# Performance work log

Measured on AMD Instinct MI355X. Metric: run time of the kernel, lower is better.

Reference implementation:

```python
import jax, jax.numpy as jnp
import numpy as np

HIDDEN = 256
ACTIONS = 8
FEAT = 256
N, T = 64, 1024


def _orthogonal(key, shape, scale):
    # hk.initializers.Orthogonal(sqrt(2)) equivalent
    n_rows, n_cols = shape
    big = max(n_rows, n_cols)
    m = jax.random.normal(key, (big, big), dtype=jnp.float32)
    q, r = jnp.linalg.qr(m)
    q = q * jnp.sign(jnp.diag(r))
    return scale * q[:n_rows, :n_cols]


def setup_inputs() -> dict:
    key = jax.random.key(0)
    ks = jax.random.split(key, 8)
    x = jax.random.normal(ks[0], (N, T, FEAT), dtype=jnp.float32)
    a = jax.random.normal(ks[1], (N, T, ACTIONS), dtype=jnp.float32)
    reset = jax.random.randint(ks[2], (N, T), 0, 2).astype(bool)
    s = np.sqrt(2).astype(np.float32)
    w_i = _orthogonal(ks[3], (FEAT, 3 * HIDDEN), s)
    w_h = _orthogonal(ks[4], (HIDDEN, 3 * HIDDEN), s)
    w_a = _orthogonal(ks[5], (ACTIONS, 3 * HIDDEN), s)
    b = jnp.zeros((3 * HIDDEN,), dtype=jnp.float32)
    initial_h = jnp.zeros((HIDDEN,), dtype=jnp.float32)
    return {"x": x, "a": a, "reset": reset, "w_i": w_i, "w_h": w_h,
            "w_a": w_a, "b": b, "initial_h": initial_h}


def reference(x, a, reset, w_i, w_h, w_a, b, initial_h):
    # x: [N,T,F], a: [N,T,A] (one-hot-like), reset: [N,T] bool
    H = initial_h.shape[0]
    w_h_z, w_h_a = w_h[:, :2 * H], w_h[:, 2 * H:]
    b_z, b_a = b[:2 * H], b[2 * H:]
    # Input-side gate projections are time-independent: precompute once.
    gx = jnp.einsum('ntf,fg->ntg', x, w_i)  # [N,T,3H]
    ga = jnp.einsum('nta,ag->ntg', a, w_a)  # [N,T,3H]
    n = x.shape[0]
    h0 = jnp.broadcast_to(initial_h[None, :], (n, H))

    def step(h, inp):
        gx_t, ga_t, r_t = inp  # [N,3H], [N,3H], [N]
        # carry sequence equals learned initial_h (learn_initial_h, is_target=False,
        # carry=None path), so reset restores the learned initial state.
        h = jnp.where(r_t[:, None], initial_h[None, :], h)
        zr = gx_t[:, :2 * H] + ga_t[:, :2 * H] + h @ w_h_z + b_z
        z, r = jnp.split(jax.nn.sigmoid(zr), 2, axis=-1)
        a_t = jnp.tanh(gx_t[:, 2 * H:] + ga_t[:, 2 * H:] + (r * h) @ w_h_a + b_a)
        h_next = (1.0 - z) * h + z * a_t
        return h_next, h_next

    xs = (jnp.swapaxes(gx, 0, 1), jnp.swapaxes(ga, 0, 1), jnp.swapaxes(reset, 0, 1))
    _, hs = jax.lax.scan(step, h0, xs)  # hs: [T,N,H]
    states = jnp.swapaxes(hs, 0, 1)     # [N,T,H]
    outputs = states                    # gru_call returns (next_state, next_state)
    return outputs, states, initial_h[None, :]
```

## Files before the change

kernel.cpp:

```cpp
#include <hip/hip_runtime.h>
#include <hip/hip_fp16.h>

#define NB 64
#define TT 1024
#define FF 256
#define HH 256
#define GG 768
#define AA 8
#define KP 288
#define MM (NB*TT)
#define SGRP 16
#define WCH 16
#define NCH (TT/WCH)
#define LDH 264
#define GSP 776

typedef _Float16 h2v __attribute__((ext_vector_type(2)));
typedef _Float16 v8h __attribute__((ext_vector_type(8)));
typedef float    v4f __attribute__((ext_vector_type(4)));

static __device__ __forceinline__ unsigned pk_rtn(float a, float b) {
    unsigned lo = (unsigned)__half_as_ushort(__float2half(a));
    unsigned hi = (unsigned)__half_as_ushort(__float2half(b));
    return lo | (hi << 16);
}
static __device__ __forceinline__ float h2f(unsigned short u) {
    return (float)__builtin_bit_cast(_Float16, u);
}
static __device__ __forceinline__ unsigned short f2h(float f) {
    return __half_as_ushort(__float2half(f));
}

__global__ __launch_bounds__(1024) void fix_reset(
    const unsigned* __restrict__ src, unsigned char* __restrict__ dst)
{
    __shared__ unsigned red[16];
    const int tid = threadIdx.x;

    unsigned acc = 0;
    #pragma unroll
    for (int i = 0; i < 16; i++)
        acc |= src[tid * 16 + i] & 0xFFFFFF00u;
    #pragma unroll
    for (int off = 32; off >= 1; off >>= 1)
        acc |= __shfl_down(acc, off, 64);
    if ((tid & 63) == 0) red[tid >> 6] = acc;
    __syncthreads();
    unsigned flag = 0;
    #pragma unroll
    for (int i = 0; i < 16; i++) flag |= red[i];
    const bool is_i32 = (flag == 0);

    if (is_i32) {
        const int per = (NB * TT) / 1024;
        #pragma unroll
        for (int i = 0; i < per; i++) {
            int idx = tid * per + i;
            dst[idx] = (unsigned char)(src[idx] != 0 ? 1 : 0);
        }
    } else {
        unsigned* d4 = (unsigned*)dst;
        #pragma unroll
        for (int i = 0; i < 16; i++)
            d4[tid * 16 + i] = src[tid * 16 + i];
    }
}

__global__ __launch_bounds__(256) void wt_build(
    const float* __restrict__ w_i, const float* __restrict__ w_a,
    const float* __restrict__ ihg, float* __restrict__ out3,
    unsigned short* __restrict__ wt)
{
    int idx = blockIdx.x * 256 + threadIdx.x;
    const int E2 = GG * KP;
    if (idx < E2) {
        int g = idx / KP, k = idx - g * KP;
        float v = 0.f;
        if (k < FF)            v = w_i[k * GG + g];
        else if (k < FF + AA)  v = w_a[(k - FF) * GG + g];
        wt[idx] = f2h(v);
    } else if (idx < E2 + HH) {
        int i = idx - E2;
        out3[i] = ihg[i];
    }
}

#define LDK 40

__global__ __launch_bounds__(256) void gemm_fused(
    const float* __restrict__ x, const float* __restrict__ a,
    const unsigned short* __restrict__ wt,
    const float* __restrict__ bias, unsigned short* __restrict__ gxa)
{
    __shared__ __align__(16) unsigned short As[128 * LDK];
    __shared__ __align__(16) unsigned short Bs[128 * LDK];

    const int bid = blockIdx.x;
    const int gt = bid % 6, mt = bid / 6;
    const int tid = threadIdx.x;
    const int lane = tid & 63, wv = tid >> 6;
    const int srow = tid & 127, shf = tid >> 7;
    const int r15 = lane & 15, q = lane >> 4;

    v4f acc[2][8];
    #pragma unroll
    for (int i = 0; i < 2; i++)
        #pragma unroll
        for (int j = 0; j < 8; j++) acc[i][j] = (v4f){0.f, 0.f, 0.f, 0.f};

    const int arow = mt * 128 + srow;

    for (int kc = 0; kc < 9; kc++) {
        uint4 A0, A1;
        if (kc < 8) {
            const float4* sp = (const float4*)(x + (size_t)arow * FF + kc * 32 + shf * 16);
            float4 f0 = sp[0], f1 = sp[1], f2 = sp[2], f3 = sp[3];
            A0.x = pk_rtn(f0.x, f0.y); A0.y = pk_rtn(f0.z, f0.w);
            A0.z = pk_rtn(f1.x, f1.y); A0.w = pk_rtn(f1.z, f1.w);
            A1.x = pk_rtn(f2.x, f2.y); A1.y = pk_rtn(f2.z, f2.w);
            A1.z = pk_rtn(f3.x, f3.y); A1.w = pk_rtn(f3.z, f3.w);
        } else if (shf == 0) {
            const float4* ap = (const float4*)(a + (size_t)arow * AA);
            float4 f0 = ap[0], f1 = ap[1];
            A0.x = pk_rtn(f0.x, f0.y); A0.y = pk_rtn(f0.z, f0.w);
            A0.z = pk_rtn(f1.x, f1.y); A0.w = pk_rtn(f1.z, f1.w);
            A1 = (uint4){0, 0, 0, 0};
        } else {
            A0 = (uint4){0, 0, 0, 0};
            A1 = (uint4){0, 0, 0, 0};
        }
        const uint4* srcB = (const uint4*)(wt + (gt * 128 + srow) * KP + kc * 32 + shf * 16);
        uint4 b0 = srcB[0], b1 = srcB[1];

        *(uint4*)(As + srow * LDK + shf * 16)     = A0;
        *(uint4*)(As + srow * LDK + shf * 16 + 8) = A1;
        *(uint4*)(Bs + srow * LDK + shf * 16)     = b0;
        *(uint4*)(Bs + srow * LDK + shf * 16 + 8) = b1;
        __syncthreads();

        v8h af[2], bf[8];
        #pragma unroll
        for (int mi = 0; mi < 2; mi++)
            af[mi] = *(const v8h*)(As + (wv * 32 + mi * 16 + r15) * LDK + q * 8);
        #pragma unroll
        for (int nj = 0; nj < 8; nj++)
            bf[nj] = *(const v8h*)(Bs + (nj * 16 + r15) * LDK + q * 8);
        #pragma unroll
        for (int mi = 0; mi < 2; mi++)
            #pragma unroll
            for (int nj = 0; nj < 8; nj++)
                acc[mi][nj] = __builtin_amdgcn_mfma_f32_16x16x32_f16(
                    af[mi], bf[nj], acc[mi][nj], 0, 0, 0);
        __syncthreads();
    }

    #pragma unroll
    for (int mi = 0; mi < 2; mi++) {
        #pragma unroll
        for (int nj = 0; nj < 8; nj++) {
            int col = gt * 128 + nj * 16 + r15;
            float bv = bias[col];
            #pragma unroll
            for (int v = 0; v < 4; v++) {
                int row = mt * 128 + wv * 32 + mi * 16 + q * 4 + v;
                float val = acc[mi][nj][v] + bv;
                gxa[row * GG + col] = f2h(val);
            }
        }
    }
}

__global__ __launch_bounds__(256) void pack_whb(
    const float* __restrict__ w_h, const unsigned char* __restrict__ rst,
    unsigned* __restrict__ whb, int* __restrict__ Ftab)
{
    const int bid = blockIdx.x;
    if (bid < 384) {
        int j = bid * 256 + threadIdx.x;
        int w    = j / 12288;
        int r    = j - w * 12288;
        int tile = r >> 8;
        int r2   = r & 255;
        int lane = r2 >> 2, d = r2 & 3;
        int r15 = lane & 15, q = lane >> 4;
        int g, k;
        if (tile < 32) {
            int nt = tile >> 3, kt = tile & 7;
            g = (nt < 2) ? (w * 32 + nt * 16 + r15)
                         : (256 + w * 32 + (nt - 2) * 16 + r15);
            k = kt * 32 + q * 8 + 2 * d;
        } else {
            int t2 = tile - 32;
            int nt2 = t2 >> 3, kt = t2 & 7;
            g = 512 + w * 32 + nt2 * 16 + r15;
            k = kt * 32 + q * 8 + 2 * d;
        }
        whb[j] = pk_rtn(w_h[k * GG + g], w_h[(k + 1) * GG + g]);
    } else {
        for (int v = threadIdx.x; v < NB * (NCH + 1); v += 256) {
            int n = v / (NCH + 1), c = v - n * (NCH + 1);
            int s = TT;
            const unsigned char* r = rst + n * TT;
            for (int t = c * WCH; t < TT; t++)
                if (r[t]) { s = t; break; }
            Ftab[v] = s;
        }
    }
}

__global__ __launch_bounds__(512, 2) void scan_mfma(
    const unsigned short* __restrict__ gxa, const uint4* __restrict__ whb4,
    const unsigned char* __restrict__ rst, const int* __restrict__ Ftab,
    const float* __restrict__ ihg, float* __restrict__ out)
{
    __shared__ __align__(16) unsigned short h16[SGRP * LDH];
    __shared__ __align__(16) unsigned short rh16[SGRP * LDH];
    __shared__ __align__(16) unsigned short gstage[2][SGRP * GSP];
    __shared__ __align__(16) uint4 waL[8 * 8 * 64];
    __shared__ int s_tb[SGRP], s_te[SGRP], s_emax;

    const int tid = threadIdx.x;
    const int w = tid >> 6, lane = tid & 63;
    const int r15 = lane & 15, q = lane >> 4;
    const int grp = blockIdx.x >> 6;
    const int c   = blockIdx.x & (NCH - 1);
    const int n0  = grp * SGRP;
    const int S   = c * WCH;

    uint4 wb[40];
    #pragma unroll
    for (int i = 0; i < 40; i++) wb[i] = whb4[(w * 48 + i) * 64 + lane];
    #pragma unroll
    for (int rr = 0; rr < 8; rr++) {
        int f = rr * 512 + tid;
        waL[f] = whb4[(rr * 48 + 40 + (tid >> 6)) * 64 + (tid & 63)];
    }

    if (tid < SGRP) {
        s_tb[tid] = (c == 0) ? 0 : Ftab[(n0 + tid) * (NCH + 1) + c];
        s_te[tid] = Ftab[(n0 + tid) * (NCH + 1) + c + 1];
    }
    if (tid == 0) {
        int m = 0;
        for (int i = 0; i < SGRP; i++) m = max(m, s_te[i]);
        s_emax = m;
    }
    for (int idx = tid; idx < SGRP * HH; idx += 512) {
        int sq = idx >> 8, jj = idx & 255;
        bool rb = (c == 0) || (rst[(n0 + sq) * TT + S] != 0);
        float v = rb ? ihg[jj] : 0.f;
        h16[sq * LDH + jj] = f2h(v);
    }
    const int seqS = tid >> 5, jS = tid & 31;
    {
        const uint4* sp = (const uint4*)(gxa + ((size_t)(n0 + seqS) * TT + S) * GG);
        uint4 g0 = sp[jS], g1 = sp[jS + 32], g2 = sp[jS + 64];
        uint4* dp = (uint4*)(gstage[0] + seqS * GSP);
        dp[jS] = g0; dp[jS + 32] = g1; dp[jS + 64] = g2;
    }
    __syncthreads();
    const int Emax = s_emax;

    const int j0 = w * 32 + r15, j1 = j0 + 16;
    const float ih0 = ihg[j0], ih1 = ihg[j1];

    int   seqi[4];
    int   tbte[4];
    float hcr[8];
    #pragma unroll
    for (int v = 0; v < 4; v++) {
        int sq = q * 4 + v;
        seqi[v] = (n0 + sq) * TT;
        tbte[v] = s_tb[sq] | (s_te[sq] << 16);
        bool rb = (c == 0) || (rst[seqi[v] + S] != 0);
        hcr[v]     = rb ? ih0 : 0.f;
        hcr[4 + v] = rb ? ih1 : 0.f;
    }

    const v4f z4 = {0.f, 0.f, 0.f, 0.f};

    for (int t = S; t < Emax; t++) {
        const int cur = (t - S) & 1, nxt = cur ^ 1;
        const int tn = (t + 1 < TT) ? (t + 1) : (TT - 1);

        uint4 g0, g1, g2;
        {
            const uint4* sp = (const uint4*)(gxa + ((size_t)(n0 + seqS) * TT + tn) * GG);
            g0 = sp[jS]; g1 = sp[jS + 32]; g2 = sp[jS + 64];
        }
        unsigned char rn[4];
        #pragma unroll
        for (int v = 0; v < 4; v++) rn[v] = rst[seqi[v] + tn];

        v4f az0 = z4, az1 = z4, ar0 = z4, ar1 = z4;
        #pragma unroll
        for (int kt = 0; kt < 8; kt++) {
            v8h af = *(const v8h*)(h16 + r15 * LDH + kt * 32 + q * 8);
            az0 = __builtin_amdgcn_mfma_f32_16x16x32_f16(af, __builtin_bit_cast(v8h, wb[kt]),      az0, 0, 0, 0);
            az1 = __builtin_amdgcn_mfma_f32_16x16x32_f16(af, __builtin_bit_cast(v8h, wb[8 + kt]),  az1, 0, 0, 0);
            ar0 = __builtin_amdgcn_mfma_f32_16x16x32_f16(af, __builtin_bit_cast(v8h, wb[16 + kt]), ar0, 0, 0, 0);
            ar1 = __builtin_amdgcn_mfma_f32_16x16x32_f16(af, __builtin_bit_cast(v8h, wb[24 + kt]), ar1, 0, 0, 0);
        }

        const unsigned short* gs = gstage[cur];
        float zs[8];
        #pragma unroll
        for (int v = 0; v < 4; v++) {
            int sq = q * 4 + v;
            int gb = sq * GSP;
            float z0 = az0[v] + h2f(gs[gb + j0]);
            float z1 = az1[v] + h2f(gs[gb + j1]);
            zs[v]     = 1.f / (1.f + __expf(-z0));
            zs[4 + v] = 1.f / (1.f + __expf(-z1));
            float r0 = ar0[v] + h2f(gs[gb + 256 + j0]);
            float r1 = ar1[v] + h2f(gs[gb + 256 + j1]);
            float s0 = 1.f / (1.f + __expf(-r0));
            float s1 = 1.f / (1.f + __expf(-r1));
            rh16[sq * LDH + j0] = f2h(s0 * hcr[v]);
            rh16[sq * LDH + j1] = f2h(s1 * hcr[4 + v]);
        }
        __syncthreads();

        v4f aa0 = z4, aa1 = z4;
        #pragma unroll
        for (int kt = 0; kt < 8; kt++) {
            v8h af = *(const v8h*)(rh16 + r15 * LDH + kt * 32 + q * 8);
            uint4 wv4 = waL[(w * 8 + kt) * 64 + lane];
            aa0 = __builtin_amdgcn_mfma_f32_16x16x32_f16(af, __builtin_bit_cast(v8h, wb[32 + kt]), aa0, 0, 0, 0);
            aa1 = __builtin_amdgcn_mfma_f32_16x16x32_f16(af, __builtin_bit_cast(v8h, wv4),         aa1, 0, 0, 0);
        }

        #pragma unroll
        for (int v = 0; v < 4; v++) {
            int sq = q * 4 + v;
            int gb = sq * GSP;
            int tb = tbte[v] & 0xFFFF, te = tbte[v] >> 16;
            bool wr = (t >= tb) && (t < te);
            int mo = (seqi[v] + t) * HH;
            float u0 = aa0[v] + h2f(gs[gb + 512 + j0]);
            float u1 = aa1[v] + h2f(gs[gb + 512 + j1]);
            float e0 = __expf(2.f * u0), e1 = __expf(2.f * u1);
            float t0 = (e0 - 1.f) / (e0 + 1.f);
            float t1 = (e1 - 1.f) / (e1 + 1.f);
            float hn0 = hcr[v]     + zs[v]     * (t0 - hcr[v]);
            float hn1 = hcr[4 + v] + zs[4 + v] * (t1 - hcr[4 + v]);
            if (wr) {
                out[mo + j0] = hn0;
                out[mo + j1] = hn1;
                out[MM * HH + mo + j0] = hn0;
                out[MM * HH + mo + j1] = hn1;
            }
            bool rb = rn[v] != 0;
            float g0f = rb ? ih0 : hn0;
            float g1f = rb ? ih1 : hn1;
            hcr[v] = g0f; hcr[4 + v] = g1f;
            h16[sq * LDH + j0] = f2h(g0f);
            h16[sq * LDH + j1] = f2h(g1f);
        }

        {
            uint4* dp = (uint4*)(gstage[nxt] + seqS * GSP);
            dp[jS] = g0; dp[jS + 32] = g1; dp[jS + 64] = g2;
        }
        __syncthreads();
    }
}

extern "C" void kernel_launch(void* const* d_in, const int* in_sizes, int n_in,
                              void* d_out, int out_size, void* d_ws, size_t ws_size,
                              hipStream_t stream)
{
    const float* x   = (const float*)d_in[0];
    const float* a   = (const float*)d_in[1];
    const void*  rsv = d_in[2];
    const float* w_i = (const float*)d_in[3];
    const float* w_h = (const float*)d_in[4];
    const float* w_a = (const float*)d_in[5];
    const float* b   = (const float*)d_in[6];
    const float* ih  = (const float*)d_in[7];
    float*       out = (float*)d_out;

    char* ws = (char*)d_ws;
    size_t o = 0;
    unsigned short* gxa  = (unsigned short*)(ws + o); o += (size_t)MM * GG * 2;
    unsigned short* wt   = (unsigned short*)(ws + o); o += (size_t)GG * KP * 2;
    unsigned char*  rst8 = (unsigned char*) (ws + o); o += (size_t)NB * TT;
    unsigned*       whb  = (unsigned*)      (ws + o); o += 98304u * 4;
    int*            Ftab = (int*)           (ws + o);

    fix_reset<<<1, 1024, 0, stream>>>((const unsigned*)rsv, rst8);

    int wtb = (GG * KP + HH + 255) / 256;
    wt_build<<<wtb, 256, 0, stream>>>(w_i, w_a, ih, out + (size_t)2 * MM * HH, wt);

    pack_whb<<<385, 256, 0, stream>>>(w_h, rst8, whb, Ftab);

    gemm_fused<<<512 * 6, 256, 0, stream>>>(x, a, wt, b, gxa);

    scan_mfma<<<(NB / SGRP) * NCH, 512, 0, stream>>>(
        gxa, (const uint4*)whb, rst8, Ftab, ih, out);
}
```

Measured before the change: 461.6 us.

## Double-buffer GEMM tiles, swizzle block order, merge prep kernels

The input-projection GEMM now double-buffers its LDS tiles. Global loads for the next K chunk are issued before the MFMA work on the current chunk, which cuts one barrier per iteration and hides load latency. Block IDs are remapped so blocks that run together, spread across the 8 XCDs, share nearby tiles. Separately, the weight-prep and w_h-packing kernels are merged into one launch, and the reset scan-table build moves into the single-block fix_reset kernel. This cuts launches at the cost of a serial Ftab build in one block and higher LDS and register use.

```diff
diff --git a/kernel.cpp b/kernel.cpp
--- a/kernel.cpp
+++ b/kernel.cpp
@@ -32,7 +32,8 @@
 }
 
 __global__ __launch_bounds__(1024) void fix_reset(
-    const unsigned* __restrict__ src, unsigned char* __restrict__ dst)
+    const unsigned* __restrict__ src, unsigned char* __restrict__ dst,
+    int* __restrict__ Ftab)
 {
     __shared__ unsigned red[16];
     const int tid = threadIdx.x;
@@ -64,119 +65,40 @@
         for (int i = 0; i < 16; i++)
             d4[tid * 16 + i] = src[tid * 16 + i];
     }
-}
-
-__global__ __launch_bounds__(256) void wt_build(
+    __syncthreads();
+
+    for (int v = tid; v < NB * (NCH + 1); v += 1024) {
+        int n = v / (NCH + 1), c = v - n * (NCH + 1);
+        int s = TT;
+        const unsigned char* r = dst + n * TT;
+        for (int t = c * WCH; t < TT; t++)
+            if (r[t]) { s = t; break; }
+        Ftab[v] = s;
+    }
+}
+
+__global__ __launch_bounds__(256) void prep_weights(
     const float* __restrict__ w_i, const float* __restrict__ w_a,
-    const float* __restrict__ ihg, float* __restrict__ out3,
-    unsigned short* __restrict__ wt)
-{
-    int idx = blockIdx.x * 256 + threadIdx.x;
-    const int E2 = GG * KP;
-    if (idx < E2) {
-        int g = idx / KP, k = idx - g * KP;
-        float v = 0.f;
-        if (k < FF)            v = w_i[k * GG + g];
-        else if (k < FF + AA)  v = w_a[(k - FF) * GG + g];
-        wt[idx] = f2h(v);
-    } else if (idx < E2 + HH) {
-        int i = idx - E2;
-        out3[i] = ihg[i];
-    }
-}
-
-#define LDK 40
-
-__global__ __launch_bounds__(256) void gemm_fused(
-    const float* __restrict__ x, const float* __restrict__ a,
-    const unsigned short* __restrict__ wt,
-    const float* __restrict__ bias, unsigned short* __restrict__ gxa)
-{
-    __shared__ __align__(16) unsigned short As[128 * LDK];
-    __shared__ __align__(16) unsigned short Bs[128 * LDK];
-
-    const int bid = blockIdx.x;
-    const int gt = bid % 6, mt = bid / 6;
-    const int tid = threadIdx.x;
-    const int lane = tid & 63, wv = tid >> 6;
-    const int srow = tid & 127, shf = tid >> 7;
-    const int r15 = lane & 15, q = lane >> 4;
-
-    v4f acc[2][8];
-    #pragma unroll
-    for (int i = 0; i < 2; i++)
-        #pragma unroll
-        for (int j = 0; j < 8; j++) acc[i][j] = (v4f){0.f, 0.f, 0.f, 0.f};
-
-    const int arow = mt * 128 + srow;
-
-    for (int kc = 0; kc < 9; kc++) {
-        uint4 A0, A1;
-        if (kc < 8) {
-            const float4* sp = (const float4*)(x + (size_t)arow * FF + kc * 32 + shf * 16);
-            float4 f0 = sp[0], f1 = sp[1], f2 = sp[2], f3 = sp[3];
-            A0.x = pk_rtn(f0.x, f0.y); A0.y = pk_rtn(f0.z, f0.w);
-            A0.z = pk_rtn(f1.x, f1.y); A0.w = pk_rtn(f1.z, f1.w);
-            A1.x = pk_rtn(f2.x, f2.y); A1.y = pk_rtn(f2.z, f2.w);
-            A1.z = pk_rtn(f3.x, f3.y); A1.w = pk_rtn(f3.z, f3.w);
-        } else if (shf == 0) {
-            const float4* ap = (const float4*)(a + (size_t)arow * AA);
-            float4 f0 = ap[0], f1 = ap[1];
-            A0.x = pk_rtn(f0.x, f0.y); A0.y = pk_rtn(f0.z, f0.w);
-            A0.z = pk_rtn(f1.x, f1.y); A0.w = pk_rtn(f1.z, f1.w);
-            A1 = (uint4){0, 0, 0, 0};
-        } else {
-            A0 = (uint4){0, 0, 0, 0};
-            A1 = (uint4){0, 0, 0, 0};
-        }
-        const uint4* srcB = (const uint4*)(wt + (gt * 128 + srow) * KP + kc * 32 + shf * 16);
-        uint4 b0 = srcB[0], b1 = srcB[1];
-
-        *(uint4*)(As + srow * LDK + shf * 16)     = A0;
-        *(uint4*)(As + srow * LDK + shf * 16 + 8) = A1;
-        *(uint4*)(Bs + srow * LDK + shf * 16)     = b0;
-        *(uint4*)(Bs + srow * LDK + shf * 16 + 8) = b1;
-        __syncthreads();
-
-        v8h af[2], bf[8];
-        #pragma unroll
-        for (int mi = 0; mi < 2; mi++)
-            af[mi] = *(const v8h*)(As + (wv * 32 + mi * 16 + r15) * LDK + q * 8);
-        #pragma unroll
-        for (int nj = 0; nj < 8; nj++)
-            bf[nj] = *(const v8h*)(Bs + (nj * 16 + r15) * LDK + q * 8);
-        #pragma unroll
-        for (int mi = 0; mi < 2; mi++)
-            #pragma unroll
-            for (int nj = 0; nj < 8; nj++)
-                acc[mi][nj] = __builtin_amdgcn_mfma_f32_16x16x32_f16(
-                    af[mi], bf[nj], acc[mi][nj], 0, 0, 0);
-        __syncthreads();
-    }
-
-    #pragma unroll
-    for (int mi = 0; mi < 2; mi++) {
-        #pragma unroll
-        for (int nj = 0; nj < 8; nj++) {
-            int col = gt * 128 + nj * 16 + r15;
-            float bv = bias[col];
-            #pragma unroll
-            for (int v = 0; v < 4; v++) {
-                int row = mt * 128 + wv * 32 + mi * 16 + q * 4 + v;
-                float val = acc[mi][nj][v] + bv;
-                gxa[row * GG + col] = f2h(val);
-            }
-        }
-    }
-}
-
-__global__ __launch_bounds__(256) void pack_whb(
-    const float* __restrict__ w_h, const unsigned char* __restrict__ rst,
-    unsigned* __restrict__ whb, int* __restrict__ Ftab)
+    const float* __restrict__ w_h, const float* __restrict__ ihg,
+    float* __restrict__ out3,
+    unsigned short* __restrict__ wt, unsigned* __restrict__ whb)
 {
     const int bid = blockIdx.x;
-    if (bid < 384) {
-        int j = bid * 256 + threadIdx.x;
+    if (bid < 865) {
+        int idx = bid * 256 + threadIdx.x;
+        const int E2 = GG * KP;
+        if (idx < E2) {
+            int g = idx / KP, k = idx - g * KP;
+            float v = 0.f;
+            if (k < FF)            v = w_i[k * GG + g];
+            else if (k < FF + AA)  v = w_a[(k - FF) * GG + g];
+            wt[idx] = f2h(v);
+        } else if (idx < E2 + HH) {
+            int i = idx - E2;
+            out3[i] = ihg[i];
+        }
+    } else {
+        int j = (bid - 865) * 256 + threadIdx.x;
         int w    = j / 12288;
         int r    = j - w * 12288;
         int tile = r >> 8;
@@ -196,14 +118,112 @@
             k = kt * 32 + q * 8 + 2 * d;
         }
         whb[j] = pk_rtn(w_h[k * GG + g], w_h[(k + 1) * GG + g]);
-    } else {
-        for (int v = threadIdx.x; v < NB * (NCH + 1); v += 256) {
-            int n = v / (NCH + 1), c = v - n * (NCH + 1);
-            int s = TT;
-            const unsigned char* r = rst + n * TT;
-            for (int t = c * WCH; t < TT; t++)
-                if (r[t]) { s = t; break; }
-            Ftab[v] = s;
+    }
+}
+
+#define LDK 40
+
+__global__ __launch_bounds__(256, 3) void gemm_fused(
+    const float* __restrict__ x, const float* __restrict__ a,
+    const unsigned short* __restrict__ wt,
+    const float* __restrict__ bias, unsigned short* __restrict__ gxa)
+{
+    __shared__ __align__(16) unsigned short As[2][128 * LDK];
+    __shared__ __align__(16) unsigned short Bs[2][128 * LDK];
+
+    const int bid = blockIdx.x;
+    const int wg  = (bid & 7) * 384 + (bid >> 3);
+    const int gt = wg % 6, mt = wg / 6;
+    const int tid = threadIdx.x;
+    const int lane = tid & 63, wv = tid >> 6;
+    const int srow = tid & 127, shf = tid >> 7;
+    const int r15 = lane & 15, q = lane >> 4;
+
+    v4f acc[2][8];
+    #pragma unroll
+    for (int i = 0; i < 2; i++)
+        #pragma unroll
+        for (int j = 0; j < 8; j++) acc[i][j] = (v4f){0.f, 0.f, 0.f, 0.f};
+
+    const int arow = mt * 128 + srow;
+    const int brow = gt * 128 + srow;
+
+    float4 f0, f1, f2, f3;
+    uint4  pb0, pb1;
+
+    auto issue = [&](int kc) {
+        if (kc < 8) {
+            const float4* sp = (const float4*)(x + (size_t)arow * FF + kc * 32 + shf * 16);
+            f0 = sp[0]; f1 = sp[1]; f2 = sp[2]; f3 = sp[3];
+        } else if (shf == 0) {
+            const float4* ap = (const float4*)(a + (size_t)arow * AA);
+            f0 = ap[0]; f1 = ap[1];
+        }
+        const uint4* srcB = (const uint4*)(wt + brow * KP + kc * 32 + shf * 16);
+        pb0 = srcB[0]; pb1 = srcB[1];
+    };
+    auto commit = [&](int buf, int kc) {
+        uint4 A0, A1;
+        if (kc < 8) {
+            A0.x = pk_rtn(f0.x, f0.y); A0.y = pk_rtn(f0.z, f0.w);
+            A0.z = pk_rtn(f1.x, f1.y); A0.w = pk_rtn(f1.z, f1.w);
+            A1.x = pk_rtn(f2.x, f2.y); A1.y = pk_rtn(f2.z, f2.w);
+            A1.z = pk_rtn(f3.x, f3.y); A1.w = pk_rtn(f3.z, f3.w);
+        } else {
+            if (shf == 0) {
+                A0.x = pk_rtn(f0.x, f0.y); A0.y = pk_rtn(f0.z, f0.w);
+                A0.z = pk_rtn(f1.x, f1.y); A0.w = pk_rtn(f1.z, f1.w);
+            } else {
+                A0 = (uint4){0, 0, 0, 0};
+            }
+            A1 = (uint4){0, 0, 0, 0};
+        }
+        *(uint4*)(As[buf] + srow * LDK + shf * 16)     = A0;
+        *(uint4*)(As[buf] + srow * LDK + shf * 16 + 8) = A1;
+        *(uint4*)(Bs[buf] + srow * LDK + shf * 16)     = pb0;
+        *(uint4*)(Bs[buf] + srow * LDK + shf * 16 + 8) = pb1;
+    };
+
+    issue(0);
+    commit(0, 0);
+    __syncthreads();
+
+    for (int kc = 0; kc < 9; kc++) {
+        const int cur = kc & 1;
+        if (kc < 8) issue(kc + 1);
+
+        v8h af[2], bf[8];
+        #pragma unroll
+        for (int mi = 0; mi < 2; mi++)
+            af[mi] = *(const v8h*)(As[cur] + (wv * 32 + mi * 16 + r15) * LDK + q * 8);
+        #pragma unroll
+        for (int nj = 0; nj < 8; nj++)
+            bf[nj] = *(const v8h*)(Bs[cur] + (nj * 16 + r15) * LDK + q * 8);
+        #pragma unroll
+        for (int mi = 0; mi < 2; mi++)
+            #pragma unroll
+            for (int nj = 0; nj < 8; nj++)
+                acc[mi][nj] = __builtin_amdgcn_mfma_f32_16x16x32_f16(
+                    af[mi], bf[nj], acc[mi][nj], 0, 0, 0);
+
+        if (kc < 8) {
+            commit(cur ^ 1, kc + 1);
+            __syncthreads();
+        }
+    }
+
+    #pragma unroll
+    for (int mi = 0; mi < 2; mi++) {
+        #pragma unroll
+        for (int nj = 0; nj < 8; nj++) {
+            int col = gt * 128 + nj * 16 + r15;
+            float bv = bias[col];
+            #pragma unroll
+            for (int v = 0; v < 4; v++) {
+                int row = mt * 128 + wv * 32 + mi * 16 + q * 4 + v;
+                float val = acc[mi][nj][v] + bv;
+                gxa[row * GG + col] = f2h(val);
+            }
         }
     }
 }
@@ -388,12 +408,10 @@
     unsigned*       whb  = (unsigned*)      (ws + o); o += 98304u * 4;
     int*            Ftab = (int*)           (ws + o);
 
-    fix_reset<<<1, 1024, 0, stream>>>((const unsigned*)rsv, rst8);
-
-    int wtb = (GG * KP + HH + 255) / 256;
-    wt_build<<<wtb, 256, 0, stream>>>(w_i, w_a, ih, out + (size_t)2 * MM * HH, wt);
-
-    pack_whb<<<385, 256, 0, stream>>>(w_h, rst8, whb, Ftab);
+    fix_reset<<<1, 1024, 0, stream>>>((const unsigned*)rsv, rst8, Ftab);
+
+    prep_weights<<<865 + 384, 256, 0, stream>>>(
+        w_i, w_a, w_h, ih, out + (size_t)2 * MM * HH, wt, whb);
 
     gemm_fused<<<512 * 6, 256, 0, stream>>>(x, a, wt, b, gxa);
 
```

Result: faster. 422.2 us (-8.5%).
